# Kernel tuning notes

Hardware: AMD Instinct MI355X
Metric: run time of the kernel (lower is better)

The kernel has to match this reference:

```python
import jax, jax.numpy as jnp
import numpy as np

D_K = 64
N_STEPS = 4
NEG = -1e9  # stand-in for -inf; keeps vjp NaN-free, numerically identical softmax


def setup_inputs() -> dict:
    key = jax.random.key(0)
    ks = jax.random.split(key, 12)
    B, N, D = 4, 2048, 1024
    s = 0.02
    return {
        "hidden": jax.random.normal(ks[0], (B, N, D), jnp.float32),
        "W1": jax.random.normal(ks[1], (64, D), jnp.float32) * s,
        "b1": jnp.zeros((64,), jnp.float32),
        "W2": jax.random.normal(ks[2], (28, 64), jnp.float32) * s,
        "b2": jnp.zeros((28,), jnp.float32),
        "Wq": jax.random.normal(ks[3], (D_K, 28), jnp.float32) * s,
        "Wk": jax.random.normal(ks[4], (D_K, 28), jnp.float32) * s,
        "Wc": jax.random.normal(ks[5], (1, 28), jnp.float32) * s,
        "bc": jnp.zeros((1,), jnp.float32),
        "Wv": jax.random.normal(ks[6], (D_K, D), jnp.float32) * s,
        "Wo": jax.random.normal(ks[7], (D, D_K), jnp.float32) * s,  # torch inits this to zeros; randomized for a non-trivial baseline
        "step_size": jnp.asarray(0.5, jnp.float32),
        "charge_decay": jnp.asarray(0.3, jnp.float32),
        "layer_idx": 0,
    }


def reference(hidden, W1, b1, W2, b2, Wq, Wk, Wc, bc, Wv, Wo, step_size, charge_decay, layer_idx):
    B, N, D = hidden.shape
    # features come from detached hidden in the torch code
    h_sg = jax.lax.stop_gradient(hidden)
    f = jax.nn.gelu(h_sg @ W1.T + b1, approximate=False)  # [B,N,64]
    features = jax.nn.sigmoid(f @ W2.T + b2)              # [B,N,28]
    Q = features @ Wq.T                                   # [B,N,64]
    K = features @ Wk.T                                   # [B,N,64]
    compat = jnp.einsum('bnd,bmd->bnm', Q, K) / jnp.float32(np.sqrt(D_K))
    charge = jax.nn.sigmoid(features @ Wc.T + bc)[..., 0]  # [B,N]
    causal = jnp.tril(jnp.ones((N, N), dtype=bool))
    logits = jnp.where(causal, compat, NEG)
    for _ in range(N_STEPS):
        attn = jax.nn.softmax(logits, axis=-1)            # [B,N,N]
        received = attn.sum(axis=-2)                      # [B,N]
        charge = charge * (1.0 - charge_decay * jax.nn.sigmoid(received - 1.0))
        energy = -compat * charge[:, :, None] * charge[:, None, :]
        logits = jnp.where(causal, logits - step_size * energy, NEG)
    attn = jax.nn.softmax(logits, axis=-1)
    V = hidden @ Wv.T                                     # [B,N,64]
    out = jnp.einsum('bnm,bmd->bnd', attn, V) @ Wo.T      # [B,N,D]
    return out * 0.1
```

## Files before the change

kernel.cpp:

```cpp
#include <hip/hip_runtime.h>
#include <hip/hip_bf16.h>

typedef unsigned short ushort_t;
typedef short bf16x8 __attribute__((ext_vector_type(8)));
typedef ushort_t u16x8 __attribute__((ext_vector_type(8)));
typedef ushort_t u16x4 __attribute__((ext_vector_type(4)));
typedef float f32x4 __attribute__((ext_vector_type(4)));

#define DEV static __device__ __forceinline__

DEV float bf2f(ushort_t u) { unsigned v = ((unsigned)u) << 16; float f; __builtin_memcpy(&f, &v, 4); return f; }
DEV short f2bf(float x) { __hip_bfloat16 h = __float2bfloat16(x); short s; __builtin_memcpy(&s, &h, 2); return s; }
DEV float sigm(float x) { return 1.0f / (1.0f + __expf(-x)); }

DEV bf16x8 cvt8(float4 a0, float4 a1) {
    bf16x8 t;
    t[0] = f2bf(a0.x); t[1] = f2bf(a0.y); t[2] = f2bf(a0.z); t[3] = f2bf(a0.w);
    t[4] = f2bf(a1.x); t[5] = f2bf(a1.y); t[6] = f2bf(a1.z); t[7] = f2bf(a1.w);
    return t;
}
DEV bf16x8 ld8f(const float* __restrict__ p) {
    return cvt8(*reinterpret_cast<const float4*>(p), *reinterpret_cast<const float4*>(p + 4));
}

__global__ void k_cvtW(const float* __restrict__ W1, const float* __restrict__ Wv,
                       ushort_t* __restrict__ Wcat) {
    int i = blockIdx.x * 256 + threadIdx.x;
    const float* src = (i < 8192) ? (W1 + (long)i * 8) : (Wv + (long)(i - 8192) * 8);
    const float4* p = reinterpret_cast<const float4*>(src);
    *reinterpret_cast<bf16x8*>(Wcat + (long)i * 8) = cvt8(p[0], p[1]);
}

__global__ __launch_bounds__(256) void k_fvfeat(const float* __restrict__ hidden,
        const ushort_t* __restrict__ Wcat, const float* __restrict__ b1,
        const float* __restrict__ W2, const float* __restrict__ b2,
        const float* __restrict__ Wq, const float* __restrict__ Wk,
        const float* __restrict__ Wc, const float* __restrict__ bc,
        ushort_t* __restrict__ Qb, ushort_t* __restrict__ Kb,
        ushort_t* __restrict__ VbT, float* __restrict__ charge0) {
    __shared__ float w2L[28 * 65], wqL[64 * 29], wkL[64 * 29], wcL[28], b2L[28];
    __shared__ float fLDS[16][65], featL[4][28];
    __shared__ __align__(16) ushort_t hLDS[16][1032];
    __shared__ float part[2][8][16][16];
    int tid = threadIdx.x;
    int m0 = blockIdx.x * 16;
    for (int i = tid; i < 28 * 64; i += 256) w2L[(i >> 6) * 65 + (i & 63)] = W2[i];
    for (int i = tid; i < 64 * 28; i += 256) {
        int r = i / 28, c = i - r * 28;
        wqL[r * 29 + c] = Wq[i];
        wkL[r * 29 + c] = Wk[i];
    }
    if (tid < 28) { wcL[tid] = Wc[tid]; b2L[tid] = b2[tid]; }
    {
        const float4* hp = reinterpret_cast<const float4*>(hidden + (long)m0 * 1024);
#pragma unroll 4
        for (int it = 0; it < 16; it++) {
            int f = it * 256 + tid;
            int row = f >> 8, colf = f & 255;
            float4 v = hp[f];
            u16x4 o;
            o[0] = (ushort_t)f2bf(v.x); o[1] = (ushort_t)f2bf(v.y);
            o[2] = (ushort_t)f2bf(v.z); o[3] = (ushort_t)f2bf(v.w);
            *reinterpret_cast<u16x4*>(&hLDS[row][colf * 4]) = o;
        }
    }
    __syncthreads();
    int wave = tid >> 6, lane = tid & 63, l16 = lane & 15, quad = lane >> 4;
    int khalf = wave >> 1, tg = wave & 1;
    f32x4 acc[4] = {};
    const ushort_t* bbase = Wcat + (long)(tg * 64 + l16) * 1024;
    {
        int kbase = khalf * 512;
#pragma unroll 2
        for (int s = 0; s < 16; s++) {
            int ko = kbase + s * 32 + quad * 8;
            bf16x8 a = *reinterpret_cast<const bf16x8*>(&hLDS[l16][ko]);
#pragma unroll
            for (int i = 0; i < 4; i++) {
                bf16x8 bfr = *reinterpret_cast<const bf16x8*>(bbase + (long)i * 16384 + ko);
                acc[i] = __builtin_amdgcn_mfma_f32_16x16x32_bf16(a, bfr, acc[i], 0, 0, 0);
            }
        }
    }
#pragma unroll
    for (int i = 0; i < 4; i++)
#pragma unroll
        for (int rr = 0; rr < 4; rr++)
            part[khalf][tg * 4 + i][quad * 4 + rr][l16] = acc[i][rr];
    __syncthreads();
    {
        int t = tid >> 5, r = (tid >> 1) & 15, ch = tid & 1;
        const float4 a0 = *reinterpret_cast<const float4*>(&part[0][t][r][ch * 8]);
        const float4 a1 = *reinterpret_cast<const float4*>(&part[0][t][r][ch * 8 + 4]);
        const float4 c0v = *reinterpret_cast<const float4*>(&part[1][t][r][ch * 8]);
        const float4 c1v = *reinterpret_cast<const float4*>(&part[1][t][r][ch * 8 + 4]);
        float v[8] = {a0.x + c0v.x, a0.y + c0v.y, a0.z + c0v.z, a0.w + c0v.w,
                      a1.x + c1v.x, a1.y + c1v.y, a1.z + c1v.z, a1.w + c1v.w};
        int colbase = t * 16 + ch * 8;
        if (t < 4) {
#pragma unroll
            for (int j = 0; j < 8; j++) {
                float x = v[j] + b1[colbase + j];
                fLDS[r][colbase + j] = 0.5f * x * (1.0f + erff(x * 0.70710678118654752f));
            }
        } else {
#pragma unroll
            for (int j = 0; j < 8; j++)
                VbT[(long)(colbase + j - 64) * 8192 + m0 + r] = (ushort_t)f2bf(v[j]);
        }
    }
    __syncthreads();
    float bcv = bc[0];
    for (int it = 0; it < 4; it++) {
        int rowl = it * 4 + wave;
        int row = m0 + rowl;
        if (lane < 28) {
            float s = b2L[lane];
#pragma unroll
            for (int j = 0; j < 64; j++) s += fLDS[rowl][j] * w2L[lane * 65 + j];
            featL[wave][lane] = sigm(s);
        }
        __syncthreads();
        float q = 0.f, k = 0.f;
#pragma unroll
        for (int i = 0; i < 28; i++) {
            float fv = featL[wave][i];
            q += fv * wqL[lane * 29 + i];
            k += fv * wkL[lane * 29 + i];
        }
        Qb[row * 64 + lane] = (ushort_t)f2bf(q * 0.125f);
        Kb[row * 64 + lane] = (ushort_t)f2bf(k);
        if (lane == 0) {
            float c = bcv;
#pragma unroll
            for (int i = 0; i < 28; i++) c += featL[wave][i] * wcL[i];
            charge0[row] = sigm(c);
        }
        __syncthreads();
    }
}

DEV void tri_decode(int r, int& ti, int& tj) {
    int t = (int)((sqrtf(8.f * (float)r + 1.f) - 1.f) * 0.5f);
    while ((t + 1) * (t + 2) / 2 <= r) t++;
    while (t * (t + 1) / 2 > r) t--;
    ti = t;
    tj = r - t * (t + 1) / 2;
}

__global__ __launch_bounds__(256) void k_compat(const ushort_t* __restrict__ Qb,
                                                const ushort_t* __restrict__ Kb,
                                                ushort_t* __restrict__ compat) {
    int bid = blockIdx.x;
    int b = bid / 136, r = bid % 136, ti, tj;
    tri_decode(r, ti, tj);
    int wave = threadIdx.x >> 6, lane = threadIdx.x & 63;
    int l16 = lane & 15, quad = lane >> 4;
    int rbase = b * 2048 + ti * 128 + wave * 32;
    int cbase = b * 2048 + tj * 128;
    f32x4 acc[2][8] = {};
#pragma unroll
    for (int kc = 0; kc < 64; kc += 32) {
        int ko = kc + quad * 8;
        bf16x8 af[2], bf[8];
#pragma unroll
        for (int f = 0; f < 2; f++)
            af[f] = *reinterpret_cast<const bf16x8*>(Qb + (long)(rbase + f * 16 + l16) * 64 + ko);
#pragma unroll
        for (int f = 0; f < 8; f++)
            bf[f] = *reinterpret_cast<const bf16x8*>(Kb + (long)(cbase + f * 16 + l16) * 64 + ko);
#pragma unroll
        for (int i = 0; i < 2; i++)
#pragma unroll
            for (int j = 0; j < 8; j++)
                acc[i][j] = __builtin_amdgcn_mfma_f32_16x16x32_bf16(af[i], bf[j], acc[i][j], 0, 0, 0);
    }
    int colt = tj * 128;
#pragma unroll
    for (int i = 0; i < 2; i++)
#pragma unroll
        for (int j = 0; j < 8; j++)
#pragma unroll
            for (int rr = 0; rr < 4; rr++) {
                long rowg = rbase + i * 16 + quad * 4 + rr;
                int col = colt + j * 16 + l16;
                compat[rowg * 2048 + col] = (ushort_t)f2bf(acc[i][j][rr]);
            }
}

template <int T>
__global__ __launch_bounds__(256, 2) void k_strip(const ushort_t* __restrict__ compat,
        const float4* __restrict__ charges4, const float* __restrict__ stepp,
        float* __restrict__ Rpart) {
    __shared__ float chR[4][8];
    __shared__ float red[4][8], Li[8];
    int bid = blockIdx.x, tid = threadIdx.x;
    int b = bid >> 8, pi = bid & 255;
    int r0A = pi * 4, r0B = 2044 - pi * 4;
    float step = stepp[0];
    if (T > 0 && tid < 8) {
        int row = (tid < 4) ? (r0A + tid) : (r0B + tid - 4);
        float4 c4 = charges4[b * 2048 + row];
        chR[0][tid] = step * c4.x;
        if (T > 1) chR[1][tid] = step * c4.y;
        if (T > 2) chR[2][tid] = step * c4.z;
        if (T > 3) chR[3][tid] = step * c4.w;
    }
    __syncthreads();
    int w = tid >> 6, lane = tid & 63;
    int c0 = tid * 4;
    const ushort_t* base = compat + (long)(b * 2048) * 2048;

    float pA[4][4] = {}, pB0[4][4] = {}, pB1[4][4] = {};
    float SA[4] = {}, SB[4] = {};

    {
        float cx[4] = {}, cy[4] = {}, cz[4] = {}, cw[4] = {};
        if (T > 0) {
#pragma unroll
            for (int k = 0; k < 4; k++) {
                float4 c = charges4[b * 2048 + c0 + k];
                cx[k] = c.x;
                if (T > 1) cy[k] = c.y;
                if (T > 2) cz[k] = c.z;
                if (T > 3) cw[k] = c.w;
            }
        }
        if (c0 <= r0A + 3) {
#pragma unroll
            for (int rr = 0; rr < 4; rr++) {
                u16x4 v = *reinterpret_cast<const u16x4*>(base + (long)(r0A + rr) * 2048 + c0);
#pragma unroll
                for (int k = 0; k < 4; k++) {
                    float sg = 1.f;
                    if (T > 0) sg += chR[0][rr] * cx[k];
                    if (T > 1) sg += chR[1][rr] * cy[k];
                    if (T > 2) sg += chR[2][rr] * cz[k];
                    if (T > 3) sg += chR[3][rr] * cw[k];
                    float p = (c0 + k <= r0A + rr) ? __expf(bf2f(v[k]) * sg) : 0.f;
                    pA[rr][k] = p;
                    SA[rr] += p;
                }
            }
        }
#pragma unroll
        for (int rr = 0; rr < 4; rr++) {
            u16x4 v = *reinterpret_cast<const u16x4*>(base + (long)(r0B + rr) * 2048 + c0);
#pragma unroll
            for (int k = 0; k < 4; k++) {
                float sg = 1.f;
                if (T > 0) sg += chR[0][4 + rr] * cx[k];
                if (T > 1) sg += chR[1][4 + rr] * cy[k];
                if (T > 2) sg += chR[2][4 + rr] * cz[k];
                if (T > 3) sg += chR[3][4 + rr] * cw[k];
                float p = __expf(bf2f(v[k]) * sg);
                pB0[rr][k] = p;
                SB[rr] += p;
            }
        }
    }
    if (1024 + c0 <= r0B + 3) {
        float cx[4] = {}, cy[4] = {}, cz[4] = {}, cw[4] = {};
        if (T > 0) {
#pragma unroll
            for (int k = 0; k < 4; k++) {
                float4 c = charges4[b * 2048 + 1024 + c0 + k];
                cx[k] = c.x;
                if (T > 1) cy[k] = c.y;
                if (T > 2) cz[k] = c.z;
                if (T > 3) cw[k] = c.w;
            }
        }
#pragma unroll
        for (int rr = 0; rr < 4; rr++) {
            u16x4 v = *reinterpret_cast<const u16x4*>(base + (long)(r0B + rr) * 2048 + 1024 + c0);
#pragma unroll
            for (int k = 0; k < 4; k++) {
                float sg = 1.f;
                if (T > 0) sg += chR[0][4 + rr] * cx[k];
                if (T > 1) sg += chR[1][4 + rr] * cy[k];
                if (T > 2) sg += chR[2][4 + rr] * cz[k];
                if (T > 3) sg += chR[3][4 + rr] * cw[k];
                float p = (1024 + c0 + k <= r0B + rr) ? __expf(bf2f(v[k]) * sg) : 0.f;
                pB1[rr][k] = p;
                SB[rr] += p;
            }
        }
    }
#pragma unroll
    for (int rr = 0; rr < 4; rr++) {
        float s = SA[rr];
        s += __shfl_xor(s, 1); s += __shfl_xor(s, 2); s += __shfl_xor(s, 4);
        s += __shfl_xor(s, 8); s += __shfl_xor(s, 16); s += __shfl_xor(s, 32);
        if (lane == 0) red[w][rr] = s;
        float t = SB[rr];
        t += __shfl_xor(t, 1); t += __shfl_xor(t, 2); t += __shfl_xor(t, 4);
        t += __shfl_xor(t, 8); t += __shfl_xor(t, 16); t += __shfl_xor(t, 32);
        if (lane == 0) red[w][4 + rr] = t;
    }
    __syncthreads();
    if (tid < 8) Li[tid] = 1.f / fmaxf(red[0][tid] + red[1][tid] + red[2][tid] + red[3][tid], 1e-30f);
    __syncthreads();
    float liA0 = Li[0], liA1 = Li[1], liA2 = Li[2], liA3 = Li[3];
    float liB0 = Li[4], liB1 = Li[5], liB2 = Li[6], liB3 = Li[7];
    float4 o0, o1;
    float* po0 = (float*)&o0;
    float* po1 = (float*)&o1;
#pragma unroll
    for (int k = 0; k < 4; k++) {
        po0[k] = pA[0][k] * liA0 + pA[1][k] * liA1 + pA[2][k] * liA2 + pA[3][k] * liA3
               + pB0[0][k] * liB0 + pB0[1][k] * liB1 + pB0[2][k] * liB2 + pB0[3][k] * liB3;
        po1[k] = pB1[0][k] * liB0 + pB1[1][k] * liB1 + pB1[2][k] * liB2 + pB1[3][k] * liB3;
    }
    *reinterpret_cast<float4*>(&Rpart[(long)bid * 2048 + c0]) = o0;
    *reinterpret_cast<float4*>(&Rpart[(long)bid * 2048 + 1024 + c0]) = o1;
}

template <int T>
__global__ __launch_bounds__(256) void k_charge(const float* __restrict__ Rpart,
        const float* __restrict__ charge0, float4* __restrict__ charges4,
        const float* __restrict__ decayp) {
    __shared__ float s8[8][33];
    int g = threadIdx.x >> 5, cl = threadIdx.x & 31;
    int m = blockIdx.x * 32 + cl;
    int b = m >> 11, col = m & 2047;
    const float* rp = Rpart + ((long)(b * 256 + g * 32) * 2048) + col;
    float s = 0.f;
#pragma unroll
    for (int i = 0; i < 32; i++) s += rp[(long)i * 2048];
    s8[g][cl] = s;
    __syncthreads();
    if (threadIdx.x < 32) {
        float t = 0.f;
#pragma unroll
        for (int gg = 0; gg < 8; gg++) t += s8[gg][threadIdx.x];
        int mm = blockIdx.x * 32 + threadIdx.x;
        float decay = decayp[0];
        float prev = (T == 1) ? charge0[mm] : ((const float*)&charges4[mm])[T - 2];
        ((float*)&charges4[mm])[T - 1] = prev * (1.f - decay * sigm(t - 1.f));
    }
}

__global__ __launch_bounds__(256, 4) void k_stripPV(const ushort_t* __restrict__ compat,
        const float4* __restrict__ charges4, const float* __restrict__ stepp,
        const ushort_t* __restrict__ VbT, ushort_t* __restrict__ Abf) {
    __shared__ float chR[4][8], red[4][8], Li[8];
    __shared__ __align__(16) ushort_t pbuf[9][1032];
    int bid = blockIdx.x, tid = threadIdx.x;
    int b = bid >> 8, pi = bid & 255;
    int r0A = pi * 4, r0B = 2044 - pi * 4;
    float step = stepp[0];
    if (tid < 8) {
        int row = (tid < 4) ? (r0A + tid) : (r0B + tid - 4);
        float4 c4 = charges4[b * 2048 + row];
        chR[0][tid] = step * c4.x; chR[1][tid] = step * c4.y;
        chR[2][tid] = step * c4.z; chR[3][tid] = step * c4.w;
    }
    u16x4 zz = {0, 0, 0, 0};
    *reinterpret_cast<u16x4*>(&pbuf[8][tid * 4]) = zz;
    __syncthreads();
    int w = tid >> 6, lane = tid & 63, l16 = lane & 15, quad = lane >> 4;
    int pr = (l16 < 8) ? l16 : 8;
    int c0 = tid * 4;
    const ushort_t* base = compat + (long)(b * 2048) * 2048;
    float S[8];
#pragma unroll
    for (int i = 0; i < 8; i++) S[i] = 0.f;
    f32x4 acc = {};

    {
        float cx[4], cy[4], cz[4], cw[4];
#pragma unroll
        for (int k = 0; k < 4; k++) {
            float4 c = charges4[b * 2048 + c0 + k];
            cx[k] = c.x; cy[k] = c.y; cz[k] = c.z; cw[k] = c.w;
        }
        if (c0 <= r0A + 3) {
#pragma unroll
            for (int i = 0; i < 4; i++) {
                u16x4 v = *reinterpret_cast<const u16x4*>(base + (long)(r0A + i) * 2048 + c0);
                u16x4 pv;
#pragma unroll
                for (int k = 0; k < 4; k++) {
                    float sg = 1.f + chR[0][i] * cx[k] + chR[1][i] * cy[k]
                                   + chR[2][i] * cz[k] + chR[3][i] * cw[k];
                    float p = (c0 + k <= r0A + i) ? __expf(bf2f(v[k]) * sg) : 0.f;
                    S[i] += p;
                    pv[k] = (ushort_t)f2bf(p);
                }
                *reinterpret_cast<u16x4*>(&pbuf[i][c0]) = pv;
            }
        } else {
#pragma unroll
            for (int i = 0; i < 4; i++) *reinterpret_cast<u16x4*>(&pbuf[i][c0]) = zz;
        }
#pragma unroll
        for (int i = 4; i < 8; i++) {
            u16x4 v = *reinterpret_cast<const u16x4*>(base + (long)(r0B + i - 4) * 2048 + c0);
            u16x4 pv;
#pragma unroll
            for (int k = 0; k < 4; k++) {
                float sg = 1.f + chR[0][i] * cx[k] + chR[1][i] * cy[k]
                               + chR[2][i] * cz[k] + chR[3][i] * cw[k];
                float p = __expf(bf2f(v[k]) * sg);
                S[i] += p;
                pv[k] = (ushort_t)f2bf(p);
            }
            *reinterpret_cast<u16x4*>(&pbuf[i][c0]) = pv;
        }
    }
    __syncthreads();
#pragma unroll 4
    for (int k0 = 0; k0 < 1024; k0 += 32) {
        bf16x8 af = *reinterpret_cast<const bf16x8*>(&pbuf[pr][k0 + quad * 8]);
        bf16x8 vf = *reinterpret_cast<const bf16x8*>(
            VbT + (long)(w * 16 + l16) * 8192 + b * 2048 + k0 + quad * 8);
        acc = __builtin_amdgcn_mfma_f32_16x16x32_bf16(af, vf, acc, 0, 0, 0);
    }
    __syncthreads();
    {
#pragma unroll
        for (int i = 0; i < 4; i++) *reinterpret_cast<u16x4*>(&pbuf[i][c0]) = zz;
        if (1024 + c0 <= r0B + 3) {
            float cx[4], cy[4], cz[4], cw[4];
#pragma unroll
            for (int k = 0; k < 4; k++) {
                float4 c = charges4[b * 2048 + 1024 + c0 + k];
                cx[k] = c.x; cy[k] = c.y; cz[k] = c.z; cw[k] = c.w;
            }
#pragma unroll
            for (int i = 4; i < 8; i++) {
                int grow = r0B + i - 4;
                u16x4 v = *reinterpret_cast<const u16x4*>(base + (long)grow * 2048 + 1024 + c0);
                u16x4 pv;
#pragma unroll
                for (int k = 0; k < 4; k++) {
                    float sg = 1.f + chR[0][i] * cx[k] + chR[1][i] * cy[k]
                                   + chR[2][i] * cz[k] + chR[3][i] * cw[k];
                    float p = (1024 + c0 + k <= grow) ? __expf(bf2f(v[k]) * sg) : 0.f;
                    S[i] += p;
                    pv[k] = (ushort_t)f2bf(p);
                }
                *reinterpret_cast<u16x4*>(&pbuf[i][c0]) = pv;
            }
        } else {
#pragma unroll
            for (int i = 4; i < 8; i++) *reinterpret_cast<u16x4*>(&pbuf[i][c0]) = zz;
        }
    }
    __syncthreads();
#pragma unroll 4
    for (int k0 = 0; k0 < 1024; k0 += 32) {
        bf16x8 af = *reinterpret_cast<const bf16x8*>(&pbuf[pr][k0 + quad * 8]);
        bf16x8 vf = *reinterpret_cast<const bf16x8*>(
            VbT + (long)(w * 16 + l16) * 8192 + b * 2048 + 1024 + k0 + quad * 8);
        acc = __builtin_amdgcn_mfma_f32_16x16x32_bf16(af, vf, acc, 0, 0, 0);
    }
#pragma unroll
    for (int i = 0; i < 8; i++) {
        float s = S[i];
        s += __shfl_xor(s, 1); s += __shfl_xor(s, 2); s += __shfl_xor(s, 4);
        s += __shfl_xor(s, 8); s += __shfl_xor(s, 16); s += __shfl_xor(s, 32);
        if (lane == 0) red[w][i] = s;
    }
    __syncthreads();
    if (tid < 8) Li[tid] = 1.f / fmaxf(red[0][tid] + red[1][tid] + red[2][tid] + red[3][tid], 1e-30f);
    __syncthreads();
    if (quad < 2) {
#pragma unroll
        for (int rr = 0; rr < 4; rr++) {
            int row8 = quad * 4 + rr;
            int grow = (row8 < 4) ? (b * 2048 + r0A + row8) : (b * 2048 + r0B + row8 - 4);
            Abf[(long)grow * 64 + w * 16 + l16] = (ushort_t)f2bf(acc[rr] * Li[row8]);
        }
    }
}

__global__ __launch_bounds__(256) void k_oproj(const ushort_t* __restrict__ Abf,
                                               const float* __restrict__ Wo,
                                               float* __restrict__ out) {
    int mt = blockIdx.x & 63, nt = blockIdx.x >> 6;
    int wave = threadIdx.x >> 6, lane = threadIdx.x & 63;
    int wm = wave >> 1, wn = wave & 1;
    int l16 = lane & 15, quad = lane >> 4;
    int row0 = mt * 128 + wm * 64;
    int col0 = nt * 128 + wn * 64;
    f32x4 acc[4][4] = {};
#pragma unroll
    for (int kc = 0; kc < 64; kc += 32) {
        int ko = kc + quad * 8;
        bf16x8 af[4], bfm[4];
#pragma unroll
        for (int f = 0; f < 4; f++)
            af[f] = *reinterpret_cast<const bf16x8*>(Abf + (long)(row0 + f * 16 + l16) * 64 + ko);
#pragma unroll
        for (int f = 0; f < 4; f++) bfm[f] = ld8f(Wo + (long)(col0 + f * 16 + l16) * 64 + ko);
#pragma unroll
        for (int i = 0; i < 4; i++)
#pragma unroll
            for (int j = 0; j < 4; j++)
                acc[i][j] = __builtin_amdgcn_mfma_f32_16x16x32_bf16(af[i], bfm[j], acc[i][j], 0, 0, 0);
    }
#pragma unroll
    for (int i = 0; i < 4; i++)
#pragma unroll
        for (int j = 0; j < 4; j++)
#pragma unroll
            for (int rr = 0; rr < 4; rr++) {
                long rowg = row0 + i * 16 + quad * 4 + rr;
                int colg = col0 + j * 16 + l16;
                out[rowg * 1024 + colg] = acc[i][j][rr] * 0.1f;
            }
}

extern "C" void kernel_launch(void* const* d_in, const int* in_sizes, int n_in,
                              void* d_out, int out_size, void* d_ws, size_t ws_size,
                              hipStream_t stream) {
    const float* hidden = (const float*)d_in[0];
    const float* W1 = (const float*)d_in[1];
    const float* b1 = (const float*)d_in[2];
    const float* W2 = (const float*)d_in[3];
    const float* b2 = (const float*)d_in[4];
    const float* Wq = (const float*)d_in[5];
    const float* Wk = (const float*)d_in[6];
    const float* Wc = (const float*)d_in[7];
    const float* bc = (const float*)d_in[8];
    const float* Wv = (const float*)d_in[9];
    const float* Wo = (const float*)d_in[10];
    const float* stepp = (const float*)d_in[11];
    const float* decayp = (const float*)d_in[12];

    char* ws = (char*)d_ws;
    size_t off = 0;
    auto alloc = [&](size_t bytes) {
        void* p = ws + off;
        off += (bytes + 255) & ~(size_t)255;
        return p;
    };
    ushort_t* compat = (ushort_t*)alloc(8192UL * 2048 * 2);
    ushort_t* Wcat = (ushort_t*)alloc(128UL * 1024 * 2);
    ushort_t* Qb = (ushort_t*)alloc(8192UL * 64 * 2);
    ushort_t* Kb = (ushort_t*)alloc(8192UL * 64 * 2);
    ushort_t* VbT = (ushort_t*)alloc(64UL * 8192 * 2);
    float* charge0 = (float*)alloc(8192UL * 4);
    float4* charges4 = (float4*)alloc(8192UL * 16);
    float* Rpart = (float*)alloc(1024UL * 2048 * 4);
    ushort_t* Abf = (ushort_t*)alloc(8192UL * 64 * 2);
    (void)ws_size; (void)in_sizes; (void)n_in; (void)out_size;

    k_cvtW<<<64, 256, 0, stream>>>(W1, Wv, Wcat);
    k_fvfeat<<<512, 256, 0, stream>>>(hidden, Wcat, b1, W2, b2, Wq, Wk, Wc, bc,
                                      Qb, Kb, VbT, charge0);
    k_compat<<<544, 256, 0, stream>>>(Qb, Kb, compat);

    k_strip<0><<<1024, 256, 0, stream>>>(compat, charges4, stepp, Rpart);
    k_charge<1><<<256, 256, 0, stream>>>(Rpart, charge0, charges4, decayp);
    k_strip<1><<<1024, 256, 0, stream>>>(compat, charges4, stepp, Rpart);
    k_charge<2><<<256, 256, 0, stream>>>(Rpart, charge0, charges4, decayp);
    k_strip<2><<<1024, 256, 0, stream>>>(compat, charges4, stepp, Rpart);
    k_charge<3><<<256, 256, 0, stream>>>(Rpart, charge0, charges4, decayp);
    k_strip<3><<<1024, 256, 0, stream>>>(compat, charges4, stepp, Rpart);
    k_charge<4><<<256, 256, 0, stream>>>(Rpart, charge0, charges4, decayp);

    k_stripPV<<<1024, 256, 0, stream>>>(compat, charges4, stepp, VbT, Abf);
    k_oproj<<<512, 256, 0, stream>>>(Abf, Wo, (float*)d_out);
}
```

Before: 254.8 us.

## Halve rows per block in feature kernel and shrink its shared memory footprint

The feature/V projection kernel now processes 8 rows per block instead of 16, launching 1024 blocks. The rows are padded to the 16-row MFMA tile with a zero row. The partial-sum buffer aliases the hidden-tile LDS, and the Wq/Wk staging in shared memory is dropped in favour of direct global reads. This cuts LDS use per block so more blocks can be resident and more CUs have work to hide the hidden-state load. The cost is that half of each MFMA tile is wasted and the W1/Wv weights are re-read by twice as many blocks.

```diff
diff --git a/kernel.cpp b/kernel.cpp
--- a/kernel.cpp
+++ b/kernel.cpp
@@ -38,23 +38,18 @@
         const float* __restrict__ Wc, const float* __restrict__ bc,
         ushort_t* __restrict__ Qb, ushort_t* __restrict__ Kb,
         ushort_t* __restrict__ VbT, float* __restrict__ charge0) {
-    __shared__ float w2L[28 * 65], wqL[64 * 29], wkL[64 * 29], wcL[28], b2L[28];
-    __shared__ float fLDS[16][65], featL[4][28];
-    __shared__ __align__(16) ushort_t hLDS[16][1032];
-    __shared__ float part[2][8][16][16];
+    __shared__ float w2L[28 * 65], wcL[28], b2L[28];
+    __shared__ float fLDS[8][65], featL[4][28];
+    __shared__ __align__(16) ushort_t hLDS[9][1032];
+    float* part = (float*)&hLDS[0][0];
     int tid = threadIdx.x;
-    int m0 = blockIdx.x * 16;
+    int m0 = blockIdx.x * 8;
     for (int i = tid; i < 28 * 64; i += 256) w2L[(i >> 6) * 65 + (i & 63)] = W2[i];
-    for (int i = tid; i < 64 * 28; i += 256) {
-        int r = i / 28, c = i - r * 28;
-        wqL[r * 29 + c] = Wq[i];
-        wkL[r * 29 + c] = Wk[i];
-    }
     if (tid < 28) { wcL[tid] = Wc[tid]; b2L[tid] = b2[tid]; }
     {
         const float4* hp = reinterpret_cast<const float4*>(hidden + (long)m0 * 1024);
 #pragma unroll 4
-        for (int it = 0; it < 16; it++) {
+        for (int it = 0; it < 8; it++) {
             int f = it * 256 + tid;
             int row = f >> 8, colf = f & 255;
             float4 v = hp[f];
@@ -63,10 +58,13 @@
             o[2] = (ushort_t)f2bf(v.z); o[3] = (ushort_t)f2bf(v.w);
             *reinterpret_cast<u16x4*>(&hLDS[row][colf * 4]) = o;
         }
+        u16x4 zz = {0, 0, 0, 0};
+        *reinterpret_cast<u16x4*>(&hLDS[8][tid * 4]) = zz;
     }
     __syncthreads();
     int wave = tid >> 6, lane = tid & 63, l16 = lane & 15, quad = lane >> 4;
     int khalf = wave >> 1, tg = wave & 1;
+    int ar = (l16 < 8) ? l16 : 8;
     f32x4 acc[4] = {};
     const ushort_t* bbase = Wcat + (long)(tg * 64 + l16) * 1024;
     {
@@ -74,7 +72,7 @@
 #pragma unroll 2
         for (int s = 0; s < 16; s++) {
             int ko = kbase + s * 32 + quad * 8;
-            bf16x8 a = *reinterpret_cast<const bf16x8*>(&hLDS[l16][ko]);
+            bf16x8 a = *reinterpret_cast<const bf16x8*>(&hLDS[ar][ko]);
 #pragma unroll
             for (int i = 0; i < 4; i++) {
                 bf16x8 bfr = *reinterpret_cast<const bf16x8*>(bbase + (long)i * 16384 + ko);
@@ -82,36 +80,36 @@
             }
         }
     }
-#pragma unroll
-    for (int i = 0; i < 4; i++)
-#pragma unroll
-        for (int rr = 0; rr < 4; rr++)
-            part[khalf][tg * 4 + i][quad * 4 + rr][l16] = acc[i][rr];
+    __syncthreads();
+    if (quad < 2) {
+#pragma unroll
+        for (int i = 0; i < 4; i++)
+#pragma unroll
+            for (int rr = 0; rr < 4; rr++)
+                part[((khalf * 8 + tg * 4 + i) * 8 + quad * 4 + rr) * 16 + l16] = acc[i][rr];
+    }
     __syncthreads();
     {
-        int t = tid >> 5, r = (tid >> 1) & 15, ch = tid & 1;
-        const float4 a0 = *reinterpret_cast<const float4*>(&part[0][t][r][ch * 8]);
-        const float4 a1 = *reinterpret_cast<const float4*>(&part[0][t][r][ch * 8 + 4]);
-        const float4 c0v = *reinterpret_cast<const float4*>(&part[1][t][r][ch * 8]);
-        const float4 c1v = *reinterpret_cast<const float4*>(&part[1][t][r][ch * 8 + 4]);
-        float v[8] = {a0.x + c0v.x, a0.y + c0v.y, a0.z + c0v.z, a0.w + c0v.w,
-                      a1.x + c1v.x, a1.y + c1v.y, a1.z + c1v.z, a1.w + c1v.w};
-        int colbase = t * 16 + ch * 8;
+        int t = tid >> 5, r = (tid >> 2) & 7, ch = tid & 3;
+        const float4 p0 = *reinterpret_cast<const float4*>(part + ((t * 8 + r) * 16 + ch * 4));
+        const float4 p1 = *reinterpret_cast<const float4*>(part + (((8 + t) * 8 + r) * 16 + ch * 4));
+        float v[4] = {p0.x + p1.x, p0.y + p1.y, p0.z + p1.z, p0.w + p1.w};
+        int colbase = t * 16 + ch * 4;
         if (t < 4) {
 #pragma unroll
-            for (int j = 0; j < 8; j++) {
+            for (int j = 0; j < 4; j++) {
                 float x = v[j] + b1[colbase + j];
                 fLDS[r][colbase + j] = 0.5f * x * (1.0f + erff(x * 0.70710678118654752f));
             }
         } else {
 #pragma unroll
-            for (int j = 0; j < 8; j++)
+            for (int j = 0; j < 4; j++)
                 VbT[(long)(colbase + j - 64) * 8192 + m0 + r] = (ushort_t)f2bf(v[j]);
         }
     }
     __syncthreads();
     float bcv = bc[0];
-    for (int it = 0; it < 4; it++) {
+    for (int it = 0; it < 2; it++) {
         int rowl = it * 4 + wave;
         int row = m0 + rowl;
         if (lane < 28) {
@@ -125,8 +123,8 @@
 #pragma unroll
         for (int i = 0; i < 28; i++) {
             float fv = featL[wave][i];
-            q += fv * wqL[lane * 29 + i];
-            k += fv * wkL[lane * 29 + i];
+            q += fv * Wq[lane * 28 + i];
+            k += fv * Wk[lane * 28 + i];
         }
         Qb[row * 64 + lane] = (ushort_t)f2bf(q * 0.125f);
         Kb[row * 64 + lane] = (ushort_t)f2bf(k);
@@ -549,8 +547,8 @@
     (void)ws_size; (void)in_sizes; (void)n_in; (void)out_size;
 
     k_cvtW<<<64, 256, 0, stream>>>(W1, Wv, Wcat);
-    k_fvfeat<<<512, 256, 0, stream>>>(hidden, Wcat, b1, W2, b2, Wq, Wk, Wc, bc,
-                                      Qb, Kb, VbT, charge0);
+    k_fvfeat<<<1024, 256, 0, stream>>>(hidden, Wcat, b1, W2, b2, Wq, Wk, Wc, bc,
+                                       Qb, Kb, VbT, charge0);
     k_compat<<<544, 256, 0, stream>>>(Qb, Kb, compat);
 
     k_strip<0><<<1024, 256, 0, stream>>>(compat, charges4, stepp, Rpart);
```

Measured after the change: 266.4 us. 1.05x slower.
